# Performance work log

Measured on AMD Instinct MI355X. Metric: run time of the kernel, lower is better.

## Reference

```python
import jax, jax.numpy as jnp
import numpy as np

H = 4           # attention heads
NEG_SLOPE = 0.2 # GATConv default leaky_relu slope
BN_EPS = 1e-5


def gat_conv(x, src, dst, W, a_src, a_dst, b, N):
    # PyG GATConv (concat=True, add_self_loops=True): self-loops appended by caller.
    C = W.shape[1] // H
    h = (x @ W).reshape(N, H, C)                      # [N,H,C]
    al_s = jnp.einsum('nhc,hc->nh', h, a_src)          # [N,H]
    al_d = jnp.einsum('nhc,hc->nh', h, a_dst)
    e = jax.nn.leaky_relu(al_s[src] + al_d[dst], NEG_SLOPE)   # [E,H]
    m = jax.ops.segment_max(e, dst, num_segments=N)            # per-dst softmax (stable)
    p = jnp.exp(e - m[dst])
    s = jax.ops.segment_sum(p, dst, num_segments=N)
    alpha = p / s[dst]                                          # [E,H]
    out = jax.ops.segment_sum(alpha[:, :, None] * h[src], dst, num_segments=N)  # [N,H,C]
    return out.reshape(N, H * C) + b


def mp_layer(x, src, dst, gw, gas, gad, gb, fw, fb, fg, fbeta, N):
    gat_out = gat_conv(x, src, dst, gw, gas, gad, gb, N)
    # feature_transform: Linear -> BatchNorm1d (eval: running_mean=0, running_var=1) -> ReLU
    y = x @ fw + fb
    y = y * (fg / jnp.sqrt(1.0 + BN_EPS)) + fbeta
    y = jax.nn.relu(y)
    return gat_out + y


def forward(x, edge_index, edge_attr, params):
    N = x.shape[0]
    loop = jnp.arange(N, dtype=edge_index.dtype)
    src = jnp.concatenate([edge_index[0], loop])   # add self loops (GATConv default)
    dst = jnp.concatenate([edge_index[1], loop])
    for p in params[:-1]:
        x = mp_layer(x, src, dst, *p, N)
        x = jax.nn.relu(x)   # dropout is identity in eval mode
    cw, cb = params[-1]
    return x @ cw + cb


def setup_inputs() -> dict:
    N, E, D, Hd, O = 80000, 1000000, 512, 128, 10
    key = jax.random.key(0)
    ks = jax.random.split(key, 40)
    ki = iter(range(40))

    def rn(shape, fan_in):
        return jax.random.normal(ks[next(ki)], shape, dtype=jnp.float32) / np.sqrt(fan_in)

    inp = {}
    inp['x'] = jax.random.normal(ks[next(ki)], (N, D), dtype=jnp.float32)
    inp['edge_index'] = jax.random.randint(ks[next(ki)], (2, E), 0, N, dtype=jnp.int64)
    inp['edge_attr'] = jax.random.uniform(ks[next(ki)], (E, 1), dtype=jnp.float32)
    dims = [D, Hd, Hd]
    for li, din in enumerate(dims):
        inp[f'l{li}_gw'] = rn((din, Hd), din)
        inp[f'l{li}_gas'] = rn((H, Hd // H), Hd // H)
        inp[f'l{li}_gad'] = rn((H, Hd // H), Hd // H)
        inp[f'l{li}_gb'] = jnp.zeros((Hd,), jnp.float32)
        inp[f'l{li}_fw'] = rn((din, Hd), din)
        inp[f'l{li}_fb'] = jnp.zeros((Hd,), jnp.float32)
        inp[f'l{li}_fg'] = jnp.ones((Hd,), jnp.float32)
        inp[f'l{li}_fbeta'] = jnp.zeros((Hd,), jnp.float32)
    inp['cls_w'] = rn((Hd, O), Hd)
    inp['cls_b'] = jnp.zeros((O,), jnp.float32)
    return inp


def reference(x, edge_index, edge_attr,
              l0_gw, l0_gas, l0_gad, l0_gb, l0_fw, l0_fb, l0_fg, l0_fbeta,
              l1_gw, l1_gas, l1_gad, l1_gb, l1_fw, l1_fb, l1_fg, l1_fbeta,
              l2_gw, l2_gas, l2_gad, l2_gb, l2_fw, l2_fb, l2_fg, l2_fbeta,
              cls_w, cls_b):
    params = [
        (l0_gw, l0_gas, l0_gad, l0_gb, l0_fw, l0_fb, l0_fg, l0_fbeta),
        (l1_gw, l1_gas, l1_gad, l1_gb, l1_fw, l1_fb, l1_fg, l1_fbeta),
        (l2_gw, l2_gas, l2_gad, l2_gb, l2_fw, l2_fb, l2_fg, l2_fbeta),
        (cls_w, cls_b),
    ]
    return forward(x, edge_index, edge_attr, params)
```

## Files before the change

### kernel.cpp

```cpp
#include <hip/hip_runtime.h>
#include <cstdint>
#include <cstddef>

#define HD 128
#define NEG_SLOPE 0.2f
#define BN_EPS 1e-5f

typedef __bf16 bf16x8 __attribute__((ext_vector_type(8)));
typedef float  f32x4  __attribute__((ext_vector_type(4)));

__device__ __forceinline__ unsigned short f2b(float f) {
    unsigned int u = __float_as_uint(f);
    u = (u + 0x7fffu + ((u >> 16) & 1u)) >> 16;
    return (unsigned short)u;
}
__device__ __forceinline__ unsigned int pack2(float lo, float hi) {
    return (unsigned int)f2b(lo) | ((unsigned int)f2b(hi) << 16);
}

__global__ void prep_w2(const float* __restrict__ gw, const float* __restrict__ fw,
                        unsigned short* __restrict__ Wt, int K)
{
    int t = blockIdx.x * 256 + threadIdx.x;
    if (t >= K * 256) return;
    int k = t >> 8, c = t & 255;
    float v = (c < 128) ? gw[(size_t)k * 128 + c] : fw[(size_t)k * 128 + (c - 128)];
    Wt[(size_t)c * K + k] = f2b(v);
}

#define GLOAD(A0, A1, B0, B1, OFF)                                            \
    A0 = *(const float4*)(xrow + (OFF));                                      \
    A1 = *(const float4*)(xrow + (OFF) + 4);                                  \
    B0 = *(const uint4*)(wrow + (OFF));                                       \
    B1 = *(const uint4*)(wrow + (OFF) + 8);

#define SUBSTEP(A0, A1, B0, B1, KNEXT)                                        \
    __syncthreads();                                                          \
    {                                                                         \
        uint4 av;                                                             \
        av.x = pack2(A0.x, A0.y); av.y = pack2(A0.z, A0.w);                   \
        av.z = pack2(A1.x, A1.y); av.w = pack2(A1.z, A1.w);                   \
        *(uint4*)(Asb + aw)      = av;                                        \
        *(uint4*)(Bsb + bw)      = B0;                                        \
        *(uint4*)(Bsb + bw + 16) = B1;                                        \
    }                                                                         \
    __syncthreads();                                                          \
    if ((KNEXT) < K) { GLOAD(A0, A1, B0, B1, (KNEXT)) }                       \
    {                                                                         \
        bf16x8 af[4], bfr[4];                                                 \
        _Pragma("unroll") for (int rt = 0; rt < 4; rt++)                      \
            af[rt] = *(const bf16x8*)(Asb + (64 * wm + rt * 16 + m) * 80 + q * 16); \
        _Pragma("unroll") for (int ct = 0; ct < 4; ct++)                      \
            bfr[ct] = *(const bf16x8*)(Bsb + (64 * wn + ct * 16 + m) * 80 + q * 16); \
        _Pragma("unroll") for (int rt = 0; rt < 4; rt++)                      \
            _Pragma("unroll") for (int ct = 0; ct < 4; ct++)                  \
                acc[rt][ct] = __builtin_amdgcn_mfma_f32_16x16x32_bf16(        \
                    af[rt], bfr[ct], acc[rt][ct], 0, 0, 0);                   \
    }

__global__ __launch_bounds__(512, 4) void gemm_dual(
    const float* __restrict__ X, const unsigned short* __restrict__ Wt,
    unsigned short* __restrict__ hb, float* __restrict__ yb, int M, int K,
    const float* __restrict__ fb, const float* __restrict__ fg,
    const float* __restrict__ fbeta, const float* __restrict__ gb)
{
    __shared__ __align__(16) char smem[128 * 80 + 256 * 80];
    char* Asb = smem;
    char* Bsb = smem + 128 * 80;

    const int tid  = threadIdx.x;
    const int row0 = blockIdx.x * 128;
    const int w    = tid >> 6, lane = tid & 63;
    const int wm   = w & 1,  wn = w >> 1;
    const int m    = lane & 15, q = lane >> 4;

    const int ra = tid >> 2, ka = (tid & 3) * 8;
    const int rb = tid >> 1, kb = (tid & 1) * 16;

    int arow = row0 + ra; if (arow >= M) arow = M - 1;

    f32x4 acc[4][4];
#pragma unroll
    for (int rt = 0; rt < 4; rt++)
#pragma unroll
        for (int ct = 0; ct < 4; ct++) acc[rt][ct] = (f32x4){0.f, 0.f, 0.f, 0.f};

    const int aw = ra * 80 + ka * 2;
    const int bw = rb * 80 + kb * 2;

    const float* xrow = X + (size_t)arow * K + ka;
    const unsigned short* wrow = Wt + (size_t)rb * K + kb;

    float4 a00, a10, a01, a11;
    uint4  b00, b10, b01, b11;
    GLOAD(a00, a10, b00, b10, 0)
    GLOAD(a01, a11, b01, b11, 32)

    for (int ks = 0; ks < K; ks += 64) {
        SUBSTEP(a00, a10, b00, b10, ks + 64)
        SUBSTEP(a01, a11, b01, b11, ks + 96)
    }

    const bool full = (row0 + 128 <= M);
    if (wn < 2) {
#pragma unroll
        for (int ct = 0; ct < 4; ct++) {
            int col = 64 * wn + ct * 16 + m;
#pragma unroll
            for (int rt = 0; rt < 4; rt++)
#pragma unroll
                for (int r = 0; r < 4; r++) {
                    int row = row0 + 64 * wm + rt * 16 + q * 4 + r;
                    if (full || row < M) hb[(size_t)row * HD + col] = f2b(acc[rt][ct][r]);
                }
        }
    } else {
        const float inv_bn = 1.0f / sqrtf(1.0f + BN_EPS);
#pragma unroll
        for (int ct = 0; ct < 4; ct++) {
            int col = 64 * (wn - 2) + ct * 16 + m;
            float g  = fg[col] * inv_bn;
            float bb = fb[col];
            float bt = fbeta[col];
            float gv = gb[col];
#pragma unroll
            for (int rt = 0; rt < 4; rt++)
#pragma unroll
                for (int r = 0; r < 4; r++) {
                    int row = row0 + 64 * wm + rt * 16 + q * 4 + r;
                    if (full || row < M) {
                        float y = (acc[rt][ct][r] + bb) * g + bt;
                        y = y > 0.f ? y : 0.f;
                        yb[(size_t)row * HD + col] = y + gv;
                    }
                }
        }
    }
}

__global__ void al_kernel(const unsigned short* __restrict__ h,
                          const float* __restrict__ a_src, const float* __restrict__ a_dst,
                          float* __restrict__ als, float* __restrict__ ald, int N)
{
    int t = blockIdx.x * blockDim.x + threadIdx.x;
    if (t >= N * 4) return;
    int n = t >> 2, hd = t & 3;
    const unsigned short* hp = h + (size_t)n * HD + hd * 32;
    const float* as = a_src + hd * 32;
    const float* ad = a_dst + hd * 32;
    float s1 = 0.f, s2 = 0.f;
#pragma unroll
    for (int i = 0; i < 32; i += 8) {
        uint4 hv = *(const uint4*)(hp + i);
        unsigned int u[4] = {hv.x, hv.y, hv.z, hv.w};
#pragma unroll
        for (int p = 0; p < 4; p++) {
            float f0 = __uint_as_float(u[p] << 16);
            float f1 = __uint_as_float(u[p] & 0xffff0000u);
            s1 += f0 * as[i + 2 * p] + f1 * as[i + 2 * p + 1];
            s2 += f0 * ad[i + 2 * p] + f1 * ad[i + 2 * p + 1];
        }
    }
    als[t] = s1; ald[t] = s2;
}

__global__ void hist_kernel(const int* __restrict__ ei, int E, int N, int* __restrict__ deg)
{
    int t = blockIdx.x * blockDim.x + threadIdx.x;
    if (t >= E + N) return;
    int d = (t < E) ? ei[E + t] : (t - E);
    atomicAdd(&deg[d], 1);
}

__global__ void scan1(const int* __restrict__ deg, int* __restrict__ rp,
                      int* __restrict__ bsum, int N)
{
    __shared__ int sh[256];
    int t = threadIdx.x;
    int i0 = blockIdx.x * 1024 + t * 4;
    int v[4];
#pragma unroll
    for (int j = 0; j < 4; j++) v[j] = (i0 + j < N) ? deg[i0 + j] : 0;
    int tot = v[0] + v[1] + v[2] + v[3];
    sh[t] = tot;
    __syncthreads();
    for (int off = 1; off < 256; off <<= 1) {
        int xv = (t >= off) ? sh[t - off] : 0;
        __syncthreads();
        sh[t] += xv;
        __syncthreads();
    }
    int run = sh[t] - tot;
    if (t == 255) bsum[blockIdx.x] = sh[255];
#pragma unroll
    for (int j = 0; j < 4; j++) {
        if (i0 + j < N) rp[i0 + j] = run;
        run += v[j];
    }
}

__global__ void scan2(int* __restrict__ bsum, int nb)
{
    if (threadIdx.x == 0 && blockIdx.x == 0) {
        int run = 0;
        for (int i = 0; i < nb; i++) { int v = bsum[i]; bsum[i] = run; run += v; }
    }
}

__global__ void scan3(int* __restrict__ rp, int* __restrict__ cur,
                      const int* __restrict__ bsum, int N, int Etot)
{
    int t = blockIdx.x * blockDim.x + threadIdx.x;
    if (t < N) {
        int v = rp[t] + bsum[t >> 10];
        rp[t] = v;
        cur[t] = v;
    } else if (t == N) {
        rp[N] = Etot;
    }
}

__global__ void scatter_kernel(const int* __restrict__ ei, int E, int N,
                               int* __restrict__ cur, int* __restrict__ col)
{
    int t = blockIdx.x * blockDim.x + threadIdx.x;
    if (t >= E + N) return;
    int s, d;
    if (t < E) { s = ei[t]; d = ei[E + t]; } else { s = t - E; d = t - E; }
    int p = atomicAdd(&cur[d], 1);
    col[p] = s;
}

__global__ __launch_bounds__(256) void agg_kernel(
    const unsigned short* __restrict__ h, const float* __restrict__ als,
    const float* __restrict__ ald, const int* __restrict__ rp,
    const int* __restrict__ col, float* __restrict__ xio, int N)
{
    int wid  = (blockIdx.x * blockDim.x + threadIdx.x) >> 6;
    int lane = threadIdx.x & 63;
    if (wid >= N) return;
    int beg = rp[wid], end = rp[wid + 1];

    int g = lane >> 4, c = lane & 15, hB = c >> 2;
    float ad_h = ald[wid * 4 + hB];
    float acc[8];
#pragma unroll
    for (int p = 0; p < 8; p++) acc[p] = 0.f;
    float wsum = 0.f;
    const unsigned short* hbase = h + c * 8;

    int j = beg + g;
    float alc = 0.f;
    uint4 hvc = (uint4){0, 0, 0, 0};
    if (j < end) {
        int s0 = col[j];
        alc = als[s0 * 4 + hB];
        hvc = *(const uint4*)(hbase + (size_t)s0 * HD);
    }
    while (j < end) {
        int jn = j + 4;
        float aln = 0.f;
        uint4 hvn = (uint4){0, 0, 0, 0};
        if (jn < end) {
            int sn = col[jn];
            aln = als[sn * 4 + hB];
            hvn = *(const uint4*)(hbase + (size_t)sn * HD);
        }
        float e = alc + ad_h;
        e = e > 0.f ? e : NEG_SLOPE * e;
        float wgt = __expf(e);
        wsum += wgt;
        unsigned int uu[4] = {hvc.x, hvc.y, hvc.z, hvc.w};
#pragma unroll
        for (int p = 0; p < 4; p++) {
            acc[2 * p]     += wgt * __uint_as_float(uu[p] << 16);
            acc[2 * p + 1] += wgt * __uint_as_float(uu[p] & 0xffff0000u);
        }
        j = jn; alc = aln; hvc = hvn;
    }
#pragma unroll
    for (int p = 0; p < 8; p++) {
        acc[p] += __shfl_xor(acc[p], 16);
        acc[p] += __shfl_xor(acc[p], 32);
    }
    wsum += __shfl_xor(wsum, 16);
    wsum += __shfl_xor(wsum, 32);
    if (g == 0) {
        float inv = 1.0f / wsum;
        float* xp = xio + (size_t)wid * HD + c * 8;
        float4 x0 = *(float4*)xp, x1 = *(float4*)(xp + 4);
        float o[8] = {acc[0] * inv + x0.x, acc[1] * inv + x0.y,
                      acc[2] * inv + x0.z, acc[3] * inv + x0.w,
                      acc[4] * inv + x1.x, acc[5] * inv + x1.y,
                      acc[6] * inv + x1.z, acc[7] * inv + x1.w};
#pragma unroll
        for (int p = 0; p < 8; p++) o[p] = o[p] > 0.f ? o[p] : 0.f;
        *(float4*)xp       = (float4){o[0], o[1], o[2], o[3]};
        *(float4*)(xp + 4) = (float4){o[4], o[5], o[6], o[7]};
    }
}

__global__ __launch_bounds__(256) void cls_kernel(
    const float* __restrict__ x, const float* __restrict__ w,
    const float* __restrict__ b, float* __restrict__ out, int N)
{
    int wid  = (blockIdx.x * blockDim.x + threadIdx.x) >> 6;
    int lane = threadIdx.x & 63;
    if (wid >= N) return;
    float x0 = x[(size_t)wid * HD + lane];
    float x1 = x[(size_t)wid * HD + 64 + lane];
    float acc[10];
#pragma unroll
    for (int o = 0; o < 10; o++)
        acc[o] = x0 * w[lane * 10 + o] + x1 * w[(lane + 64) * 10 + o];
#pragma unroll
    for (int o = 0; o < 10; o++) {
        float v = acc[o];
#pragma unroll
        for (int off = 1; off < 64; off <<= 1) v += __shfl_xor(v, off);
        acc[o] = v;
    }
    float v = 0.f;
#pragma unroll
    for (int o = 0; o < 10; o++) if (lane == o) v = acc[o];
    if (lane < 10) out[(size_t)wid * 10 + lane] = v + b[lane];
}

extern "C" void kernel_launch(void* const* d_in, const int* in_sizes, int n_in,
                              void* d_out, int out_size, void* d_ws, size_t ws_size,
                              hipStream_t stream)
{
    const float* x0 = (const float*)d_in[0];
    const int*   ei = (const int*)d_in[1];
    const int N = in_sizes[0] / 512;
    const int E = in_sizes[1] / 2;
    const int Etot = E + N;

    const float *gw[3], *gas[3], *gad[3], *gbp[3], *fw[3], *fbp[3], *fgp[3], *fbt[3];
    for (int l = 0; l < 3; l++) {
        int b = 3 + 8 * l;
        gw[l]  = (const float*)d_in[b + 0];
        gas[l] = (const float*)d_in[b + 1];
        gad[l] = (const float*)d_in[b + 2];
        gbp[l] = (const float*)d_in[b + 3];
        fw[l]  = (const float*)d_in[b + 4];
        fbp[l] = (const float*)d_in[b + 5];
        fgp[l] = (const float*)d_in[b + 6];
        fbt[l] = (const float*)d_in[b + 7];
    }
    const float* cw = (const float*)d_in[27];
    const float* cb = (const float*)d_in[28];

    char* p = (char*)d_ws;
    auto carve = [&](size_t bytes) -> char* {
        char* r = p; p += (bytes + 255) & ~(size_t)255; return r;
    };
    float* xA   = (float*)carve((size_t)N * HD * 4);
    float* xB   = (float*)carve((size_t)N * HD * 4);
    unsigned short* hbuf = (unsigned short*)carve((size_t)N * HD * 2);
    float* als  = (float*)carve((size_t)N * 4 * 4);
    float* ald  = (float*)carve((size_t)N * 4 * 4);
    int* rp   = (int*)carve((size_t)(N + 1) * 4);
    int* deg  = (int*)carve((size_t)N * 4);
    int* cur  = (int*)carve((size_t)N * 4);
    int* bsum = (int*)carve(4096);
    int* col  = (int*)carve((size_t)Etot * 4);
    unsigned short* wT[3];
    for (int l = 0; l < 3; l++) {
        int K = (l == 0) ? 512 : HD;
        wT[l] = (unsigned short*)carve((size_t)256 * K * 2);
    }

    for (int l = 0; l < 3; l++) {
        int K = (l == 0) ? 512 : HD;
        int nt = K * 256;
        prep_w2<<<(nt + 255) / 256, 256, 0, stream>>>(gw[l], fw[l], wT[l], K);
    }

    hipMemsetAsync(deg, 0, (size_t)N * 4, stream);
    hist_kernel<<<(Etot + 255) / 256, 256, 0, stream>>>(ei, E, N, deg);
    int nb = (N + 1023) / 1024;
    scan1<<<nb, 256, 0, stream>>>(deg, rp, bsum, N);
    scan2<<<1, 64, 0, stream>>>(bsum, nb);
    scan3<<<(N + 256) / 256, 256, 0, stream>>>(rp, cur, bsum, N, Etot);
    scatter_kernel<<<(Etot + 255) / 256, 256, 0, stream>>>(ei, E, N, cur, col);

    for (int l = 0; l < 3; l++) {
        const float* xin = (l == 0) ? x0 : ((l == 1) ? xA : xB);
        float* xout = (l == 1) ? xB : xA;
        int K = (l == 0) ? 512 : HD;
        int mblocks = (N + 127) / 128;
        gemm_dual<<<mblocks, 512, 0, stream>>>(xin, wT[l], hbuf, xout, N, K,
                                               fbp[l], fgp[l], fbt[l], gbp[l]);
        al_kernel<<<(N * 4 + 255) / 256, 256, 0, stream>>>(hbuf, gas[l], gad[l], als, ald, N);
        agg_kernel<<<(N + 3) / 4, 256, 0, stream>>>(hbuf, als, ald, rp, col, xout, N);
    }

    cls_kernel<<<(N + 3) / 4, 256, 0, stream>>>(xA, cw, cb, (float*)d_out, N);
}
```

Measured before the change: 871.2 us.

## Double-buffer LDS tiles in dual GEMM to halve barriers per k-step

Replaces the single LDS tile with two ping-pong buffers, each holding an A and a B tile. Global loads for the next k-slice are issued before the MFMA compute on the current buffer, and their LDS write goes to the other buffer, so each 32-wide substep needs one barrier instead of two. The cost is double the shared memory per block (about 60 KB), which may lower occupancy from the 4 blocks per CU requested in launch bounds. It also carries only one set of prefetch registers instead of two, which shortens how far ahead global loads run.

Measured after the change: 776.5 us. 10.9% less time.

```diff
diff --git a/kernel.cpp b/kernel.cpp
--- a/kernel.cpp
+++ b/kernel.cpp
@@ -28,30 +28,29 @@
     Wt[(size_t)c * K + k] = f2b(v);
 }
 
-#define GLOAD(A0, A1, B0, B1, OFF)                                            \
-    A0 = *(const float4*)(xrow + (OFF));                                      \
-    A1 = *(const float4*)(xrow + (OFF) + 4);                                  \
-    B0 = *(const uint4*)(wrow + (OFF));                                       \
-    B1 = *(const uint4*)(wrow + (OFF) + 8);
-
-#define SUBSTEP(A0, A1, B0, B1, KNEXT)                                        \
-    __syncthreads();                                                          \
+#define GLOAD(OFF)                                                            \
+    pa0 = *(const float4*)(xrow + (OFF));                                     \
+    pa1 = *(const float4*)(xrow + (OFF) + 4);                                 \
+    pb0 = *(const uint4*)(wrow + (OFF));                                      \
+    pb1 = *(const uint4*)(wrow + (OFF) + 8);
+
+#define DSWR(BUF)                                                             \
     {                                                                         \
         uint4 av;                                                             \
-        av.x = pack2(A0.x, A0.y); av.y = pack2(A0.z, A0.w);                   \
-        av.z = pack2(A1.x, A1.y); av.w = pack2(A1.z, A1.w);                   \
-        *(uint4*)(Asb + aw)      = av;                                        \
-        *(uint4*)(Bsb + bw)      = B0;                                        \
-        *(uint4*)(Bsb + bw + 16) = B1;                                        \
-    }                                                                         \
-    __syncthreads();                                                          \
-    if ((KNEXT) < K) { GLOAD(A0, A1, B0, B1, (KNEXT)) }                       \
+        av.x = pack2(pa0.x, pa0.y); av.y = pack2(pa0.z, pa0.w);               \
+        av.z = pack2(pa1.x, pa1.y); av.w = pack2(pa1.z, pa1.w);               \
+        *(uint4*)((BUF) + aw)              = av;                              \
+        *(uint4*)((BUF) + 10240 + bw)      = pb0;                             \
+        *(uint4*)((BUF) + 10240 + bw + 16) = pb1;                             \
+    }
+
+#define COMPUTE(BUF)                                                          \
     {                                                                         \
         bf16x8 af[4], bfr[4];                                                 \
         _Pragma("unroll") for (int rt = 0; rt < 4; rt++)                      \
-            af[rt] = *(const bf16x8*)(Asb + (64 * wm + rt * 16 + m) * 80 + q * 16); \
+            af[rt] = *(const bf16x8*)((BUF) + (64 * wm + rt * 16 + m) * 80 + q * 16); \
         _Pragma("unroll") for (int ct = 0; ct < 4; ct++)                      \
-            bfr[ct] = *(const bf16x8*)(Bsb + (64 * wn + ct * 16 + m) * 80 + q * 16); \
+            bfr[ct] = *(const bf16x8*)((BUF) + 10240 + (64 * wn + ct * 16 + m) * 80 + q * 16); \
         _Pragma("unroll") for (int rt = 0; rt < 4; rt++)                      \
             _Pragma("unroll") for (int ct = 0; ct < 4; ct++)                  \
                 acc[rt][ct] = __builtin_amdgcn_mfma_f32_16x16x32_bf16(        \
@@ -64,9 +63,9 @@
     const float* __restrict__ fb, const float* __restrict__ fg,
     const float* __restrict__ fbeta, const float* __restrict__ gb)
 {
-    __shared__ __align__(16) char smem[128 * 80 + 256 * 80];
-    char* Asb = smem;
-    char* Bsb = smem + 128 * 80;
+    __shared__ __align__(16) char smem[2 * 30720];
+    char* buf0 = smem;
+    char* buf1 = smem + 30720;
 
     const int tid  = threadIdx.x;
     const int row0 = blockIdx.x * 128;
@@ -91,14 +90,22 @@
     const float* xrow = X + (size_t)arow * K + ka;
     const unsigned short* wrow = Wt + (size_t)rb * K + kb;
 
-    float4 a00, a10, a01, a11;
-    uint4  b00, b10, b01, b11;
-    GLOAD(a00, a10, b00, b10, 0)
-    GLOAD(a01, a11, b01, b11, 32)
+    float4 pa0, pa1;
+    uint4  pb0, pb1;
+
+    GLOAD(0)
+    DSWR(buf0)
+    __syncthreads();
 
     for (int ks = 0; ks < K; ks += 64) {
-        SUBSTEP(a00, a10, b00, b10, ks + 64)
-        SUBSTEP(a01, a11, b01, b11, ks + 96)
+        GLOAD(ks + 32)
+        COMPUTE(buf0)
+        DSWR(buf1)
+        __syncthreads();
+        if (ks + 64 < K) { GLOAD(ks + 64) }
+        COMPUTE(buf1)
+        if (ks + 64 < K) { DSWR(buf0) }
+        __syncthreads();
     }
 
     const bool full = (row0 + 128 <= M);
```
